# Optimization experiments

Hardware: AMD Instinct MI355X
Metric: run time of the kernel (lower is better)

The kernel has to match this reference:

```python
import jax, jax.numpy as jnp
import numpy as np

EPS = 1e-5

def conv1d(x, w, b, pad):
    # x: [N, Cin, T], w: [Cout, Cin, K]
    y = jax.lax.conv_general_dilated(x, w, (1,), [(pad, pad)],
                                     dimension_numbers=("NCH", "OIH", "NCH"))
    return y + b[None, :, None]

def bn_eval(x, gamma, beta, mean, var):
    # BatchNorm1d in inference mode over channel dim of [N, C, T]
    inv = gamma / jnp.sqrt(var + EPS)
    return x * inv[None, :, None] + (beta - mean * inv)[None, :, None]

def setup_inputs() -> dict:
    key = jax.random.key(0)
    ks = jax.random.split(key, 16)
    B, E, N, T = 8, 16, 64, 128
    D, OUT = 32, 64  # timeseries_dim, output_dim
    inp = {
        "node_features": jax.random.normal(ks[0], (B, E, N, T, 1), dtype=jnp.float32),
        "edge_features": jax.random.normal(ks[1], (B, E, T), dtype=jnp.float32),
        "conv1_w": jax.random.normal(ks[2], (D, 1, 3), dtype=jnp.float32) * 0.3,
        "conv1_b": jax.random.normal(ks[3], (D,), dtype=jnp.float32) * 0.1,
        "conv2_w": jax.random.normal(ks[4], (1, D, 3), dtype=jnp.float32) * 0.1,
        "conv2_b": jax.random.normal(ks[5], (1,), dtype=jnp.float32) * 0.1,
        "conv3_w": jax.random.normal(ks[6], (OUT, 1, 1), dtype=jnp.float32) * 0.3,
        "conv3_b": jax.random.normal(ks[7], (OUT,), dtype=jnp.float32) * 0.1,
        "bn1_gamma": jax.random.uniform(ks[8], (D,), dtype=jnp.float32) + 0.5,
        "bn1_beta": jax.random.normal(ks[9], (D,), dtype=jnp.float32) * 0.1,
        "bn1_mean": jax.random.normal(ks[10], (D,), dtype=jnp.float32) * 0.1,
        "bn1_var": jax.random.uniform(ks[11], (D,), dtype=jnp.float32) + 0.5,
        "bn2_gamma": jax.random.uniform(ks[12], (1,), dtype=jnp.float32) + 0.5,
        "bn2_beta": jax.random.normal(ks[13], (1,), dtype=jnp.float32) * 0.1,
        "bn2_mean": jax.random.normal(ks[14], (1,), dtype=jnp.float32) * 0.1,
        "bn2_var": jax.random.uniform(ks[15], (1,), dtype=jnp.float32) + 0.5,
    }
    return inp

def reference(node_features, edge_features, conv1_w, conv1_b, conv2_w, conv2_b,
              conv3_w, conv3_b, bn1_gamma, bn1_beta, bn1_mean, bn1_var,
              bn2_gamma, bn2_beta, bn2_mean, bn2_var):
    B, E, N, T, _ = node_features.shape
    OUT = conv3_w.shape[0]
    # Self-connectivity: each (b,e,n) node processes its own [1,1,T] series and
    # the sum over its (single) connected edge is the identity. Fuse the triple
    # python loop into one batched conv pipeline over B*E*N series.
    x = node_features.reshape(B * E * N, 1, T)          # [BEN, 1, T]
    x = jax.nn.relu(bn_eval(conv1d(x, conv1_w, conv1_b, 1),
                            bn1_gamma, bn1_beta, bn1_mean, bn1_var))  # [BEN, D, T]
    x = jax.nn.relu(bn_eval(conv1d(x, conv2_w, conv2_b, 1),
                            bn2_gamma, bn2_beta, bn2_mean, bn2_var))  # [BEN, 1, T]
    x = conv1d(x, conv3_w, conv3_b, 0)                  # [BEN, OUT, T]
    return x.reshape(B, E, N, OUT, T)
```

## Files before the change

### kernel.cpp

```cpp
#include <hip/hip_runtime.h>

#define EPSF 1e-5f


__global__ __launch_bounds__(128) void hnc_kernel(
    const float* __restrict__ x_in,
    const float* __restrict__ w1,
    const float* __restrict__ b1,
    const float* __restrict__ w2,
    const float* __restrict__ b2,
    const float* __restrict__ w3,
    const float* __restrict__ b3,
    const float* __restrict__ g1, const float* __restrict__ be1,
    const float* __restrict__ m1, const float* __restrict__ v1,
    const float* __restrict__ g2, const float* __restrict__ be2,
    const float* __restrict__ m2, const float* __restrict__ v2,
    float* __restrict__ out)
{
    const int T = 128, OUT = 64;

    __shared__ float x_s[130];
    __shared__ float y1_s[32 * 130];
    __shared__ float y2_s[128];
    __shared__ float a1_s[3][32];
    __shared__ float c1_s[32];
    __shared__ float w2_s[3][32];
    __shared__ float w3_s[64];
    __shared__ float b3_s[64];

    const int tid = threadIdx.x;
    const int series = blockIdx.x;

    x_s[1 + tid] = x_in[(size_t)series * T + tid];
    if (tid == 0) { x_s[0] = 0.f; x_s[129] = 0.f; }
    if (tid < 32) {
        float inv = g1[tid] * rsqrtf(v1[tid] + EPSF);
        a1_s[0][tid] = inv * w1[tid * 3 + 0];
        a1_s[1][tid] = inv * w1[tid * 3 + 1];
        a1_s[2][tid] = inv * w1[tid * 3 + 2];
        c1_s[tid] = b1[tid] * inv + be1[tid] - m1[tid] * inv;
    } else if (tid < 64) {
        int d = tid - 32;
        float s2 = g2[0] * rsqrtf(v2[0] + EPSF);
        w2_s[0][d] = s2 * w2[d * 3 + 0];
        w2_s[1][d] = s2 * w2[d * 3 + 1];
        w2_s[2][d] = s2 * w2[d * 3 + 2];
    }
    if (tid < 64) {
        w3_s[tid] = w3[tid];
        b3_s[tid] = b3[tid];
        int d = tid >> 1;
        y1_s[d * 130 + (tid & 1) * 129] = 0.f;
    }
    __syncthreads();

    float xm = x_s[tid], x0 = x_s[tid + 1], xp = x_s[tid + 2];
    #pragma unroll
    for (int d = 0; d < 32; ++d) {
        float v = a1_s[0][d] * xm + a1_s[1][d] * x0 + a1_s[2][d] * xp + c1_s[d];
        y1_s[d * 130 + 1 + tid] = fmaxf(v, 0.f);
    }
    __syncthreads();

    float s2 = g2[0] * rsqrtf(v2[0] + EPSF);
    float c2 = b2[0] * s2 + be2[0] - m2[0] * s2;
    float acc = c2;
    #pragma unroll
    for (int d = 0; d < 32; ++d) {
        const float* row = &y1_s[d * 130 + tid];
        acc += w2_s[0][d] * row[0] + w2_s[1][d] * row[1] + w2_s[2][d] * row[2];
    }
    y2_s[tid] = fmaxf(acc, 0.f);
    __syncthreads();

    float4* out4 = (float4*)(out + (size_t)series * OUT * T);
    #pragma unroll
    for (int i = 0; i < 16; ++i) {
        int flat4 = i * 128 + tid;
        int o = flat4 >> 5;
        int t = (flat4 << 2) & 127;
        float4 y = *(const float4*)&y2_s[t];
        float w = w3_s[o], b = b3_s[o];
        out4[flat4] = make_float4(fmaf(w, y.x, b), fmaf(w, y.y, b),
                                  fmaf(w, y.z, b), fmaf(w, y.w, b));
    }
}

extern "C" void kernel_launch(void* const* d_in, const int* in_sizes, int n_in,
                              void* d_out, int out_size, void* d_ws, size_t ws_size,
                              hipStream_t stream) {
    const float* x   = (const float*)d_in[0];
    const float* w1  = (const float*)d_in[2];
    const float* b1  = (const float*)d_in[3];
    const float* w2  = (const float*)d_in[4];
    const float* b2  = (const float*)d_in[5];
    const float* w3  = (const float*)d_in[6];
    const float* b3  = (const float*)d_in[7];
    const float* g1  = (const float*)d_in[8];
    const float* be1 = (const float*)d_in[9];
    const float* m1  = (const float*)d_in[10];
    const float* v1  = (const float*)d_in[11];
    const float* g2  = (const float*)d_in[12];
    const float* be2 = (const float*)d_in[13];
    const float* m2  = (const float*)d_in[14];
    const float* v2  = (const float*)d_in[15];

    const int T = 128;
    const int n_series = in_sizes[0] / T;

    hnc_kernel<<<n_series, 128, 0, stream>>>(x, w1, b1, w2, b2, w3, b3,
                                             g1, be1, m1, v1, g2, be2, m2, v2,
                                             (float*)d_out);
}
```

Before: 54.39 us.

## Fuse conv1 into conv2 via recompute and use nontemporal output stores

Each thread now recomputes the three neighbouring conv1+BN+ReLU values it needs and folds them straight into the conv2 accumulators. This removes the 32x130 shared-memory intermediate and one barrier, at the cost of about three times the conv1 arithmetic. Edge handling is done with masks on the first and last timestep. The output write, which is the dominant traffic, now uses nontemporal vector stores to avoid cache pollution.

```diff
diff --git a/kernel.cpp b/kernel.cpp
--- a/kernel.cpp
+++ b/kernel.cpp
@@ -1,6 +1,8 @@
 #include <hip/hip_runtime.h>
 
 #define EPSF 1e-5f
+
+typedef float f32x4 __attribute__((ext_vector_type(4)));
 
 
 __global__ __launch_bounds__(128) void hnc_kernel(
@@ -19,20 +21,22 @@
 {
     const int T = 128, OUT = 64;
 
-    __shared__ float x_s[130];
-    __shared__ float y1_s[32 * 130];
+    __shared__ float x_s[132];
     __shared__ float y2_s[128];
     __shared__ float a1_s[3][32];
     __shared__ float c1_s[32];
-    __shared__ float w2_s[3][32];
+    __shared__ float w2f_s[3][32];
     __shared__ float w3_s[64];
     __shared__ float b3_s[64];
+    __shared__ float c2_s;
 
     const int tid = threadIdx.x;
     const int series = blockIdx.x;
 
-    x_s[1 + tid] = x_in[(size_t)series * T + tid];
-    if (tid == 0) { x_s[0] = 0.f; x_s[129] = 0.f; }
+    x_s[2 + tid] = x_in[(size_t)series * T + tid];
+    if (tid < 2) x_s[tid] = 0.f;
+    else if (tid < 4) x_s[128 + tid] = 0.f;
+
     if (tid < 32) {
         float inv = g1[tid] * rsqrtf(v1[tid] + EPSF);
         a1_s[0][tid] = inv * w1[tid * 3 + 0];
@@ -42,47 +46,54 @@
     } else if (tid < 64) {
         int d = tid - 32;
         float s2 = g2[0] * rsqrtf(v2[0] + EPSF);
-        w2_s[0][d] = s2 * w2[d * 3 + 0];
-        w2_s[1][d] = s2 * w2[d * 3 + 1];
-        w2_s[2][d] = s2 * w2[d * 3 + 2];
-    }
-    if (tid < 64) {
-        w3_s[tid] = w3[tid];
-        b3_s[tid] = b3[tid];
-        int d = tid >> 1;
-        y1_s[d * 130 + (tid & 1) * 129] = 0.f;
+        w2f_s[0][d] = s2 * w2[d * 3 + 0];
+        w2f_s[1][d] = s2 * w2[d * 3 + 1];
+        w2f_s[2][d] = s2 * w2[d * 3 + 2];
+        if (d == 0) c2_s = b2[0] * s2 + be2[0] - m2[0] * s2;
+    } else if (tid < 128) {
+        int o = tid - 64;
+        w3_s[o] = w3[o];
+        b3_s[o] = b3[o];
     }
     __syncthreads();
 
-    float xm = x_s[tid], x0 = x_s[tid + 1], xp = x_s[tid + 2];
+    const float xm2 = x_s[tid];
+    const float xm1 = x_s[tid + 1];
+    const float x0  = x_s[tid + 2];
+    const float xp1 = x_s[tid + 3];
+    const float xp2 = x_s[tid + 4];
+
+    float accm = 0.f, acc0 = 0.f, accp = 0.f;
     #pragma unroll
     for (int d = 0; d < 32; ++d) {
-        float v = a1_s[0][d] * xm + a1_s[1][d] * x0 + a1_s[2][d] * xp + c1_s[d];
-        y1_s[d * 130 + 1 + tid] = fmaxf(v, 0.f);
+        const float a0 = a1_s[0][d], a1 = a1_s[1][d], a2 = a1_s[2][d];
+        const float c  = c1_s[d];
+        float ym = fmaxf(fmaf(a0, xm2, fmaf(a1, xm1, fmaf(a2, x0,  c))), 0.f);
+        float y0 = fmaxf(fmaf(a0, xm1, fmaf(a1, x0,  fmaf(a2, xp1, c))), 0.f);
+        float yp = fmaxf(fmaf(a0, x0,  fmaf(a1, xp1, fmaf(a2, xp2, c))), 0.f);
+        accm = fmaf(w2f_s[0][d], ym, accm);
+        acc0 = fmaf(w2f_s[1][d], y0, acc0);
+        accp = fmaf(w2f_s[2][d], yp, accp);
     }
+    const float mm = (tid == 0)   ? 0.f : 1.f;
+    const float mp = (tid == 127) ? 0.f : 1.f;
+    y2_s[tid] = fmaxf(fmaf(mm, accm, fmaf(mp, accp, acc0 + c2_s)), 0.f);
     __syncthreads();
 
-    float s2 = g2[0] * rsqrtf(v2[0] + EPSF);
-    float c2 = b2[0] * s2 + be2[0] - m2[0] * s2;
-    float acc = c2;
-    #pragma unroll
-    for (int d = 0; d < 32; ++d) {
-        const float* row = &y1_s[d * 130 + tid];
-        acc += w2_s[0][d] * row[0] + w2_s[1][d] * row[1] + w2_s[2][d] * row[2];
-    }
-    y2_s[tid] = fmaxf(acc, 0.f);
-    __syncthreads();
-
-    float4* out4 = (float4*)(out + (size_t)series * OUT * T);
+    f32x4* out4 = (f32x4*)(out + (size_t)series * OUT * T);
     #pragma unroll
     for (int i = 0; i < 16; ++i) {
         int flat4 = i * 128 + tid;
         int o = flat4 >> 5;
         int t = (flat4 << 2) & 127;
-        float4 y = *(const float4*)&y2_s[t];
+        f32x4 y = *(const f32x4*)&y2_s[t];
         float w = w3_s[o], b = b3_s[o];
-        out4[flat4] = make_float4(fmaf(w, y.x, b), fmaf(w, y.y, b),
-                                  fmaf(w, y.z, b), fmaf(w, y.w, b));
+        f32x4 r;
+        r.x = fmaf(w, y.x, b);
+        r.y = fmaf(w, y.y, b);
+        r.z = fmaf(w, y.z, b);
+        r.w = fmaf(w, y.w, b);
+        __builtin_nontemporal_store(r, &out4[flat4]);
     }
 }
 
```

Result: slower. 57.64 us (+6.0%).
